# Optimization experiments

Hardware: AMD Instinct MI355X
Metric: run time of the kernel (lower is better)

Reference implementation:

```python
import jax, jax.numpy as jnp
import numpy as np

N = 2800        # real node count (before hardcoded pad)
NPAD = 3000     # module pads node dim to 3000
F_IN = 8192     # node_features
H1 = 256        # dim_h1 (GCLSTM in_channels)
H2 = 128        # GCLSTM out_channels
E = 179200      # edges (avg degree 64)


def setup_inputs() -> dict:
    key = jax.random.key(0)
    ks = jax.random.split(key, 12)
    inp = {
        "x": jax.random.normal(ks[0], (N, F_IN), jnp.float32),
        "edge_index": jax.random.randint(ks[1], (2, E), 0, N, dtype=jnp.int64),
        "edge_weight": jax.random.uniform(ks[2], (E,), jnp.float32),
        "h0": jax.random.normal(ks[3], (NPAD, H2), jnp.float32),
        "c0": jax.random.normal(ks[4], (NPAD, H2), jnp.float32),
        # fc0: node_features -> dim_h1
        "fc0_w": jax.random.normal(ks[5], (F_IN, H1), jnp.float32) / np.float32(np.sqrt(F_IN)),
        "fc0_b": jnp.zeros((H1,), jnp.float32),
        # GCLSTM gate params, stacked over gates [i, f, c, o]
        "Wx": jax.random.normal(ks[6], (4, H1, H2), jnp.float32) / np.float32(np.sqrt(H1)),
        "bg": jnp.zeros((4, H2), jnp.float32),
        # ChebConv (K=2) weights per gate: theta_0, theta_1, bias
        "cw0": jax.random.normal(ks[7], (4, H2, H2), jnp.float32) / np.float32(np.sqrt(H2)),
        "cw1": jax.random.normal(ks[8], (4, H2, H2), jnp.float32) / np.float32(np.sqrt(H2)),
        "cb": jnp.zeros((4, H2), jnp.float32),
        # final fc: 128 -> 1
        "fc_w": jax.random.normal(ks[9], (H2, 1), jnp.float32) / np.float32(np.sqrt(H2)),
        "fc_b": jnp.zeros((1,), jnp.float32),
    }
    return inp


def _cheb_scaled_laplacian(edge_index, edge_weight, num_nodes):
    # ChebConv 'sym' norm with lambda_max=2: L_hat = -D^{-1/2} A D^{-1/2}
    # (diagonal of scaled Laplacian cancels to zero with fill_value=-1 self loops)
    row, col = edge_index[0], edge_index[1]
    deg = jax.ops.segment_sum(edge_weight, row, num_segments=num_nodes)
    dinv = jnp.where(deg > 0, jax.lax.rsqrt(jnp.where(deg > 0, deg, 1.0)), 0.0)
    return -dinv[row] * edge_weight * dinv[col]  # per-edge weight of L_hat


def reference(x, edge_weight, h0, c0, fc0_w, fc0_b, Wx, bg, cw0, cw1, cb,
              fc_w, fc_b, edge_index):
    n_real = x.shape[0]
    # hardcoded zero-padding of node dim to 3000
    xp = jnp.concatenate([x, jnp.zeros((NPAD - n_real, x.shape[1]), x.dtype)], axis=0)
    z = jax.nn.relu(xp @ fc0_w + fc0_b)                       # [3000, 256]

    row, col = edge_index[0], edge_index[1]
    w_hat = _cheb_scaled_laplacian(edge_index, edge_weight, NPAD)
    # Chebyshev T1 term: L_hat @ H  (shared across all four gates)
    T1 = jax.ops.segment_sum(w_hat[:, None] * h0[row], col, num_segments=NPAD)  # [3000,128]

    # all four gate pre-activations at once: X W_x + ChebConv(H) + b
    gates = (jnp.einsum('nf,gfo->gno', z, Wx)
             + jnp.einsum('nd,gdo->gno', h0, cw0)
             + jnp.einsum('nd,gdo->gno', T1, cw1)
             + (bg + cb)[:, None, :])                          # [4, 3000, 128]

    i = jax.nn.sigmoid(gates[0])
    f = jax.nn.sigmoid(gates[1])
    t = jnp.tanh(gates[2])
    o = jax.nn.sigmoid(gates[3])
    c_new = f * c0 + i * t
    h_new = o * jnp.tanh(c_new)                                # [3000, 128]

    out = (jax.nn.relu(h_new) @ fc_w + fc_b)[:, 0]             # squeeze last dim
    out = out[:n_real]                                         # drop padding rows
    return out, h_new
```

## Files before the change

kernel.cpp:

```cpp
#include <hip/hip_runtime.h>
#include <math.h>

#define N_REAL 2800
#define NPAD   3000
#define F_IN   8192
#define H1     256
#define H2     128
#define NE     179200
#define UDIM   512
#define NGATE  512
#define MPAD   3072
#define SPLITK 16
#define KCH    (F_IN / SPLITK)

typedef _Float16 half8_t __attribute__((ext_vector_type(8)));
typedef _Float16 half4_t __attribute__((ext_vector_type(4)));
typedef float    floatx4 __attribute__((ext_vector_type(4)));

__device__ __forceinline__ void async_g2l_16(const _Float16* g, _Float16* l) {
    __builtin_amdgcn_global_load_lds(
        (const __attribute__((address_space(1))) unsigned int*)g,
        (__attribute__((address_space(3))) unsigned int*)l, 16, 0, 0);
}

__global__ __launch_bounds__(256)
void prep_kernel(const float* __restrict__ w, const float* __restrict__ Wx,
                 const float* __restrict__ cw0, const float* __restrict__ cw1,
                 const float* __restrict__ bg, const float* __restrict__ cb,
                 const float* __restrict__ h0,
                 _Float16* __restrict__ wTp, _Float16* __restrict__ Wcp,
                 float* __restrict__ biasv, float* __restrict__ deg,
                 int* __restrict__ counts, _Float16* __restrict__ U16) {
    int b = blockIdx.x;
    if (b < 2048) {
        __shared__ float tile[32][33];
        int k0 = (b & 255) * 32;
        int n0 = (b >> 8) * 32;
        int tx = threadIdx.x & 31, ty = threadIdx.x >> 5;
#pragma unroll
        for (int r = 0; r < 4; r++)
            tile[ty + r * 8][tx] = w[(size_t)(k0 + ty + r * 8) * H1 + n0 + tx];
        __syncthreads();
        int t = threadIdx.x;
        if (t < 128) {
            int u_l = t >> 5;
            int n_l = t & 31;
            half8_t h;
#pragma unroll
            for (int j = 0; j < 8; j++) h[j] = (_Float16)tile[u_l * 8 + j][n_l];
            *(half8_t*)&wTp[(((size_t)(k0 >> 3) + u_l) * H1 + n0 + n_l) * 8] = h;
        }
    } else if (b < 3072) {
        int idx = (b - 2048) * 256 + threadIdx.x;
        if (idx < UDIM * NGATE) {
            int col = idx >> 9;
            int f   = idx & 511;
            int g = col >> 7, o = col & 127;
            float v;
            if (f < H1)            v = Wx[((size_t)g * H1 + f) * H2 + o];
            else if (f < H1 + H2)  v = cw0[((size_t)g * H2 + (f - H1)) * H2 + o];
            else                   v = cw1[((size_t)g * H2 + (f - H1 - H2)) * H2 + o];
            Wcp[(((size_t)(f >> 3)) * NGATE + col) * 8 + (f & 7)] = (_Float16)v;
            if (f == 0) biasv[col] = bg[col] + cb[col];
        }
    } else if (b < 3096) {
        int i = (b - 3072) * 256 + threadIdx.x;
        if (i < NPAD) deg[i] = 0.f;
        else { int j = i - NPAD; if (j < 3072) counts[j] = 0; }
    } else {
        int q = (b - 3096) * 256 + threadIdx.x;
        int m = q >> 5;
        int o4 = (q & 31) * 4;
        half4_t h = {};
        if (m < NPAD) {
            float4 v = *(const float4*)&h0[(size_t)m * H2 + o4];
            h[0] = (_Float16)v.x; h[1] = (_Float16)v.y; h[2] = (_Float16)v.z; h[3] = (_Float16)v.w;
        }
        *(half4_t*)&U16[(size_t)m * UDIM + H1 + o4] = h;
    }
}

__global__ __launch_bounds__(256, 3)
void g1hist_kernel(const float* __restrict__ x, const _Float16* __restrict__ wTp,
                   const int* __restrict__ ei, const float* __restrict__ ew,
                   float* __restrict__ P, float* __restrict__ deg,
                   int* __restrict__ counts) {
    __shared__ __align__(16) _Float16 As[8][64][8];
    __shared__ __align__(16) _Float16 Bs[8][256][8];
    const int b = blockIdx.x;
    const int t = threadIdx.x;
    if (b < 700) {
        int e = b * 256 + t;
        if (e < NE) {
            int r = ei[e];
            int c = ei[NE + e];
            atomicAdd(&deg[r], ew[e]);
            atomicAdd(&counts[c], 1);
        }
        return;
    }
    const int lin = b - 700;
    const int sk  = lin & 15;
    const int mb  = lin >> 4;
    const int wave = t >> 6, lane = t & 63;
    const int l16 = lane & 15, u4 = lane >> 4;
    const int m0 = mb * 64;
    const int kbase = sk * KCH;

    const int arow = t >> 2;
    const int aseg = t & 3;
    const bool avalid = (m0 + arow) < N_REAL;
    const float* agp = x + (size_t)(m0 + arow) * F_IN + kbase + aseg * 16;

    floatx4 acc[4][4] = {};

    float4 a0 = make_float4(0.f, 0.f, 0.f, 0.f), a1 = a0, a2 = a0, a3 = a0;
    if (avalid) {
        a0 = *(const float4*)(agp + 0);
        a1 = *(const float4*)(agp + 4);
        a2 = *(const float4*)(agp + 8);
        a3 = *(const float4*)(agp + 12);
    }

    for (int kk = 0; kk < KCH; kk += 64) {
        const _Float16* bbase = wTp + ((size_t)((kbase + kk) >> 3)) * (H1 * 8);
#pragma unroll
        for (int q = 0; q < 2; q++) {
            int u = wave * 2 + q;
#pragma unroll
            for (int rg = 0; rg < 4; rg++)
                async_g2l_16(bbase + ((size_t)u * H1 + rg * 64 + lane) * 8,
                             &Bs[u][rg * 64 + lane][0]);
        }
        half8_t hlo, hhi;
        hlo[0] = (_Float16)a0.x; hlo[1] = (_Float16)a0.y; hlo[2] = (_Float16)a0.z; hlo[3] = (_Float16)a0.w;
        hlo[4] = (_Float16)a1.x; hlo[5] = (_Float16)a1.y; hlo[6] = (_Float16)a1.z; hlo[7] = (_Float16)a1.w;
        hhi[0] = (_Float16)a2.x; hhi[1] = (_Float16)a2.y; hhi[2] = (_Float16)a2.z; hhi[3] = (_Float16)a2.w;
        hhi[4] = (_Float16)a3.x; hhi[5] = (_Float16)a3.y; hhi[6] = (_Float16)a3.z; hhi[7] = (_Float16)a3.w;
        *(half8_t*)&As[aseg * 2][arow][0]     = hlo;
        *(half8_t*)&As[aseg * 2 + 1][arow][0] = hhi;
        __syncthreads();
        if (kk + 64 < KCH && avalid) {
            a0 = *(const float4*)(agp + kk + 64);
            a1 = *(const float4*)(agp + kk + 68);
            a2 = *(const float4*)(agp + kk + 72);
            a3 = *(const float4*)(agp + kk + 76);
        }
#pragma unroll
        for (int ks = 0; ks < 2; ks++) {
            half8_t a[4], bfr[4];
#pragma unroll
            for (int i = 0; i < 4; i++) a[i] = *(const half8_t*)&As[ks * 4 + u4][i * 16 + l16][0];
#pragma unroll
            for (int j = 0; j < 4; j++) bfr[j] = *(const half8_t*)&Bs[ks * 4 + u4][wave * 64 + j * 16 + l16][0];
#pragma unroll
            for (int i = 0; i < 4; i++)
#pragma unroll
                for (int j = 0; j < 4; j++)
                    acc[i][j] = __builtin_amdgcn_mfma_f32_16x16x32_f16(a[i], bfr[j], acc[i][j], 0, 0, 0);
        }
        __syncthreads();
    }

    float* Pb = P + ((size_t)sk * MPAD + m0) * H1;
#pragma unroll
    for (int i = 0; i < 4; i++)
#pragma unroll
        for (int j = 0; j < 4; j++) {
            int n = wave * 64 + j * 16 + l16;
#pragma unroll
            for (int r = 0; r < 4; r++)
                Pb[(size_t)(i * 16 + u4 * 4 + r) * H1 + n] = acc[i][j][r];
        }
}

__device__ __forceinline__ void zreduce_body(int zb, int t, const float* __restrict__ P,
                                             const float* __restrict__ fc0_b,
                                             _Float16* __restrict__ U16) {
    int q = zb * 256 + t;
    int m = q >> 6;
    int n4 = (q & 63) * 4;
    float s0 = 0.f, s1 = 0.f, s2 = 0.f, s3 = 0.f;
#pragma unroll
    for (int sk = 0; sk < SPLITK; sk++) {
        float4 p = *(const float4*)&P[((size_t)sk * MPAD + m) * H1 + n4];
        s0 += p.x; s1 += p.y; s2 += p.z; s3 += p.w;
    }
    float4 bb = *(const float4*)&fc0_b[n4];
    half4_t h;
    h[0] = (_Float16)fmaxf(s0 + bb.x, 0.f);
    h[1] = (_Float16)fmaxf(s1 + bb.y, 0.f);
    h[2] = (_Float16)fmaxf(s2 + bb.z, 0.f);
    h[3] = (_Float16)fmaxf(s3 + bb.w, 0.f);
    *(half4_t*)&U16[(size_t)m * UDIM + n4] = h;
}

__global__ __launch_bounds__(256)
void scanz_kernel(const int* __restrict__ counts, int* __restrict__ offsets,
                  const float* __restrict__ deg, float* __restrict__ dinv,
                  int* __restrict__ cursor, const float* __restrict__ P,
                  const float* __restrict__ fc0_b, _Float16* __restrict__ U16) {
    int b = blockIdx.x;
    int t = threadIdx.x;
    if (b == 0) {
        __shared__ int wt[4];
        int i0 = t * 12;
        int v[12];
        int s = 0;
#pragma unroll
        for (int j = 0; j < 12; j++) { v[j] = counts[i0 + j]; s += v[j]; }
        int incl = s;
#pragma unroll
        for (int d = 1; d < 64; d <<= 1) {
            int n = __shfl_up(incl, d);
            if ((t & 63) >= d) incl += n;
        }
        if ((t & 63) == 63) wt[t >> 6] = incl;
        __syncthreads();
        int wbase = 0;
#pragma unroll
        for (int w = 0; w < 4; w++) wbase += (w < (t >> 6)) ? wt[w] : 0;
        int run = wbase + incl - s;
#pragma unroll
        for (int j = 0; j < 12; j++) {
            offsets[i0 + j] = run;
            cursor[i0 + j]  = run;
            run += v[j];
        }
        for (int i = t; i < NPAD; i += 256) {
            float d = deg[i];
            dinv[i] = (d > 0.f) ? rsqrtf(d) : 0.f;
        }
    } else {
        zreduce_body(b - 1, t, P, fc0_b, U16);
    }
}

__global__ __launch_bounds__(256)
void scatz_kernel(const int* __restrict__ ei, int* __restrict__ cursor,
                  int* __restrict__ eid, const float* __restrict__ P,
                  const float* __restrict__ fc0_b, _Float16* __restrict__ U16) {
    int b = blockIdx.x;
    int t = threadIdx.x;
    if (b < 700) {
        int e = b * 256 + t;
        if (e < NE) {
            int c = ei[NE + e];
            int p = atomicAdd(&cursor[c], 1);
            eid[p] = e;
        }
    } else {
        zreduce_body(384 + (b - 700), t, P, fc0_b, U16);
    }
}

__global__ __launch_bounds__(128)
void gather_kernel(const int* __restrict__ ei, const float* __restrict__ ew,
                   const float* __restrict__ h0, const float* __restrict__ dinv,
                   const int* __restrict__ offsets, const int* __restrict__ eid,
                   _Float16* __restrict__ U16) {
    __shared__ int   sr[128];
    __shared__ float sw[128];
    int n = blockIdx.x;
    int t = threadIdx.x;
    int beg = offsets[n], end = offsets[n + 1];
    float dc = dinv[n];
    float acc = 0.f;
    for (int base = beg; base < end; base += 128) {
        int j = base + t;
        if (j < end) {
            int e = eid[j];
            int r = ei[e];
            sr[t] = r;
            sw[t] = -dinv[r] * ew[e];
        }
        __syncthreads();
        int cnt = min(128, end - base);
        int k = 0;
        for (; k + 8 <= cnt; k += 8) {
            int   r0 = sr[k],   r1 = sr[k+1], r2 = sr[k+2], r3 = sr[k+3];
            int   r4 = sr[k+4], r5 = sr[k+5], r6 = sr[k+6], r7 = sr[k+7];
            float w0 = sw[k],   w1 = sw[k+1], w2 = sw[k+2], w3 = sw[k+3];
            float w4 = sw[k+4], w5 = sw[k+5], w6 = sw[k+6], w7 = sw[k+7];
            float v0 = h0[(size_t)r0 * H2 + t];
            float v1 = h0[(size_t)r1 * H2 + t];
            float v2 = h0[(size_t)r2 * H2 + t];
            float v3 = h0[(size_t)r3 * H2 + t];
            float v4 = h0[(size_t)r4 * H2 + t];
            float v5 = h0[(size_t)r5 * H2 + t];
            float v6 = h0[(size_t)r6 * H2 + t];
            float v7 = h0[(size_t)r7 * H2 + t];
            acc += w0 * v0 + w1 * v1 + w2 * v2 + w3 * v3
                 + w4 * v4 + w5 * v5 + w6 * v6 + w7 * v7;
        }
        for (; k < cnt; k++)
            acc += sw[k] * h0[(size_t)sr[k] * H2 + t];
        __syncthreads();
    }
    U16[(size_t)n * UDIM + H1 + H2 + t] = (_Float16)(acc * dc);
}

__global__ __launch_bounds__(256, 3)
void gemm2_mfma(const _Float16* __restrict__ U16, const _Float16* __restrict__ Wcp,
                float* __restrict__ gatesP) {
    __shared__ __align__(16) _Float16 As[8][64][8];
    __shared__ __align__(16) _Float16 Bs[8][256][8];
    const int t = threadIdx.x;
    const int wave = t >> 6, lane = t & 63;
    const int l16 = lane & 15, u4 = lane >> 4;
    const int n0 = blockIdx.x * 256;
    const int m0 = blockIdx.y * 64;
    const int kz = blockIdx.z * 256;

    floatx4 acc[4][4] = {};

    for (int kk = kz; kk < kz + 256; kk += 64) {
        const _Float16* bbase = Wcp + ((size_t)(kk >> 3)) * (NGATE * 8);
#pragma unroll
        for (int q = 0; q < 2; q++) {
            int u = wave * 2 + q;
            async_g2l_16(U16 + (size_t)(m0 + lane) * UDIM + kk + u * 8, &As[u][lane][0]);
#pragma unroll
            for (int rg = 0; rg < 4; rg++)
                async_g2l_16(bbase + ((size_t)u * NGATE + n0 + rg * 64 + lane) * 8,
                             &Bs[u][rg * 64 + lane][0]);
        }
        __syncthreads();
#pragma unroll
        for (int ks = 0; ks < 2; ks++) {
            half8_t a[4], bfr[4];
#pragma unroll
            for (int i = 0; i < 4; i++) a[i] = *(const half8_t*)&As[ks * 4 + u4][i * 16 + l16][0];
#pragma unroll
            for (int j = 0; j < 4; j++) bfr[j] = *(const half8_t*)&Bs[ks * 4 + u4][wave * 64 + j * 16 + l16][0];
#pragma unroll
            for (int i = 0; i < 4; i++)
#pragma unroll
                for (int j = 0; j < 4; j++)
                    acc[i][j] = __builtin_amdgcn_mfma_f32_16x16x32_f16(a[i], bfr[j], acc[i][j], 0, 0, 0);
        }
        __syncthreads();
    }

    float* g = gatesP + (size_t)blockIdx.z * MPAD * NGATE;
#pragma unroll
    for (int i = 0; i < 4; i++)
#pragma unroll
        for (int j = 0; j < 4; j++) {
            int n = n0 + wave * 64 + j * 16 + l16;
#pragma unroll
            for (int r = 0; r < 4; r++)
                g[(size_t)(m0 + i * 16 + u4 * 4 + r) * NGATE + n] = acc[i][j][r];
        }
}

__global__ __launch_bounds__(128)
void lstm_kernel(const float* __restrict__ gates, const float* __restrict__ c0,
                 const float* __restrict__ biasv, const float* __restrict__ fc_w,
                 const float* __restrict__ fc_b, float* __restrict__ out) {
    __shared__ float red[2];
    int n = blockIdx.x;
    int o = threadIdx.x;
    const float* g0 = gates + (size_t)n * NGATE;
    const float* g1 = g0 + (size_t)MPAD * NGATE;
    float gi = g0[o]          + g1[o]          + biasv[o];
    float gf = g0[H2 + o]     + g1[H2 + o]     + biasv[H2 + o];
    float gt = g0[2 * H2 + o] + g1[2 * H2 + o] + biasv[2 * H2 + o];
    float go = g0[3 * H2 + o] + g1[3 * H2 + o] + biasv[3 * H2 + o];
    float iv = 1.f / (1.f + expf(-gi));
    float fv = 1.f / (1.f + expf(-gf));
    float tv = tanhf(gt);
    float ov = 1.f / (1.f + expf(-go));
    float c = fv * c0[(size_t)n * H2 + o] + iv * tv;
    float h = ov * tanhf(c);
    out[N_REAL + (size_t)n * H2 + o] = h;

    float r = fmaxf(h, 0.f) * fc_w[o];
#pragma unroll
    for (int s = 32; s; s >>= 1) r += __shfl_down(r, s);
    if ((o & 63) == 0) red[o >> 6] = r;
    __syncthreads();
    if (o == 0 && n < N_REAL) out[n] = red[0] + red[1] + fc_b[0];
}

extern "C" void kernel_launch(void* const* d_in, const int* in_sizes, int n_in,
                              void* d_out, int out_size, void* d_ws, size_t ws_size,
                              hipStream_t stream) {
    const float* x     = (const float*)d_in[0];
    const int*   ei    = (const int*)d_in[1];
    const float* ew    = (const float*)d_in[2];
    const float* h0    = (const float*)d_in[3];
    const float* c0    = (const float*)d_in[4];
    const float* fc0_w = (const float*)d_in[5];
    const float* fc0_b = (const float*)d_in[6];
    const float* Wx    = (const float*)d_in[7];
    const float* bg    = (const float*)d_in[8];
    const float* cw0   = (const float*)d_in[9];
    const float* cw1   = (const float*)d_in[10];
    const float* cb    = (const float*)d_in[11];
    const float* fc_w  = (const float*)d_in[12];
    const float* fc_b  = (const float*)d_in[13];
    float* out = (float*)d_out;

    float* P      = (float*)d_ws;
    float* gates  = P + (size_t)SPLITK * MPAD * H1;
    float* biasv  = gates + 2 * (size_t)MPAD * NGATE;
    float* deg    = biasv + NGATE;
    float* dinv   = deg + NPAD;
    int*   counts = (int*)(dinv + NPAD);
    int*   offs   = counts + 3072;
    int*   cursor = offs + 3072;
    int*   eid    = cursor + 3072;
    _Float16* U16 = (_Float16*)(((uintptr_t)(eid + NE) + 255) & ~(uintptr_t)255);
    _Float16* Wcp = U16 + (size_t)MPAD * UDIM;
    _Float16* wTp = Wcp + (size_t)UDIM * NGATE;

    prep_kernel<<<3480, 256, 0, stream>>>(fc0_w, Wx, cw0, cw1, bg, cb, h0, wTp, Wcp, biasv, deg, counts, U16);
    g1hist_kernel<<<700 + (MPAD / 64) * SPLITK, 256, 0, stream>>>(x, wTp, ei, ew, P, deg, counts);
    scanz_kernel<<<385, 256, 0, stream>>>(counts, offs, deg, dinv, cursor, P, fc0_b, U16);
    scatz_kernel<<<1084, 256, 0, stream>>>(ei, cursor, eid, P, fc0_b, U16);
    gather_kernel<<<NPAD, 128, 0, stream>>>(ei, ew, h0, dinv, offs, eid, U16);
    gemm2_mfma<<<dim3(NGATE / 256, MPAD / 64, 2), 256, 0, stream>>>(U16, Wcp, gates);
    lstm_kernel<<<NPAD, 128, 0, stream>>>(gates, c0, biasv, fc_w, fc_b, out);
}
```

Baseline: 270.2 us.

## Privatize edge histograms in LDS and overlap gather with partial gate GEMM

Degree and count histograms are now built by eight blocks using shared-memory atomics and written out as per-block partials, which removes the deg/counts zeroing and the global atomics. The CSR scatter then uses per-block LDS cursors built from the prefix sums. The gate GEMM is split by K: the z and h0 part (K 0..384) runs in the same launch as the T1 gather, and a small second kernel handles the T1 columns. The gather now uses 256 threads that split the edges into two halves. The risks are that only 8 blocks do the histogram and scatter work, so those phases have little parallelism, and the eid order inside each segment changes.

```diff
diff --git a/kernel.cpp b/kernel.cpp
--- a/kernel.cpp
+++ b/kernel.cpp
@@ -12,10 +12,15 @@
 #define MPAD   3072
 #define SPLITK 16
 #define KCH    (F_IN / SPLITK)
+#define NHB    8
+#define EPB    (NE / NHB)
 
 typedef _Float16 half8_t __attribute__((ext_vector_type(8)));
 typedef _Float16 half4_t __attribute__((ext_vector_type(4)));
 typedef float    floatx4 __attribute__((ext_vector_type(4)));
+
+typedef _Float16 AsT[64][8];
+typedef _Float16 BsT[256][8];
 
 __device__ __forceinline__ void async_g2l_16(const _Float16* g, _Float16* l) {
     __builtin_amdgcn_global_load_lds(
@@ -29,8 +34,7 @@
                  const float* __restrict__ bg, const float* __restrict__ cb,
                  const float* __restrict__ h0,
                  _Float16* __restrict__ wTp, _Float16* __restrict__ Wcp,
-                 float* __restrict__ biasv, float* __restrict__ deg,
-                 int* __restrict__ counts, _Float16* __restrict__ U16) {
+                 float* __restrict__ biasv, _Float16* __restrict__ U16) {
     int b = blockIdx.x;
     if (b < 2048) {
         __shared__ float tile[32][33];
@@ -63,12 +67,8 @@
             Wcp[(((size_t)(f >> 3)) * NGATE + col) * 8 + (f & 7)] = (_Float16)v;
             if (f == 0) biasv[col] = bg[col] + cb[col];
         }
-    } else if (b < 3096) {
-        int i = (b - 3072) * 256 + threadIdx.x;
-        if (i < NPAD) deg[i] = 0.f;
-        else { int j = i - NPAD; if (j < 3072) counts[j] = 0; }
     } else {
-        int q = (b - 3096) * 256 + threadIdx.x;
+        int q = (b - 3072) * 256 + threadIdx.x;
         int m = q >> 5;
         int o4 = (q & 31) * 4;
         half4_t h = {};
@@ -83,23 +83,32 @@
 __global__ __launch_bounds__(256, 3)
 void g1hist_kernel(const float* __restrict__ x, const _Float16* __restrict__ wTp,
                    const int* __restrict__ ei, const float* __restrict__ ew,
-                   float* __restrict__ P, float* __restrict__ deg,
-                   int* __restrict__ counts) {
-    __shared__ __align__(16) _Float16 As[8][64][8];
-    __shared__ __align__(16) _Float16 Bs[8][256][8];
+                   float* __restrict__ P, int* __restrict__ cnt_p,
+                   float* __restrict__ deg_p) {
+    __shared__ __align__(16) char smem[40960];
     const int b = blockIdx.x;
     const int t = threadIdx.x;
-    if (b < 700) {
-        int e = b * 256 + t;
-        if (e < NE) {
-            int r = ei[e];
-            int c = ei[NE + e];
-            atomicAdd(&deg[r], ew[e]);
-            atomicAdd(&counts[c], 1);
+    if (b < NHB) {
+        float* sdeg = (float*)smem;
+        int*   scnt = (int*)(smem + 12288);
+        for (int i = t; i < 3072; i += 256) { sdeg[i] = 0.f; scnt[i] = 0; }
+        __syncthreads();
+        int e0 = b * EPB;
+        for (int i = t; i < EPB; i += 256) {
+            int e = e0 + i;
+            atomicAdd(&sdeg[ei[e]], ew[e]);
+            atomicAdd(&scnt[ei[NE + e]], 1);
+        }
+        __syncthreads();
+        for (int i = t; i < 3072; i += 256) {
+            deg_p[b * 3072 + i] = sdeg[i];
+            cnt_p[b * 3072 + i] = scnt[i];
         }
         return;
     }
-    const int lin = b - 700;
+    AsT* As = reinterpret_cast<AsT*>(smem);
+    BsT* Bs = reinterpret_cast<BsT*>(smem + 8192);
+    const int lin = b - NHB;
     const int sk  = lin & 15;
     const int mb  = lin >> 4;
     const int wave = t >> 6, lane = t & 63;
@@ -196,10 +205,10 @@
 }
 
 __global__ __launch_bounds__(256)
-void scanz_kernel(const int* __restrict__ counts, int* __restrict__ offsets,
-                  const float* __restrict__ deg, float* __restrict__ dinv,
-                  int* __restrict__ cursor, const float* __restrict__ P,
-                  const float* __restrict__ fc0_b, _Float16* __restrict__ U16) {
+void scanz_kernel(const int* __restrict__ cnt_p, const float* __restrict__ deg_p,
+                  int* __restrict__ offsets, float* __restrict__ dinv,
+                  const float* __restrict__ P, const float* __restrict__ fc0_b,
+                  _Float16* __restrict__ U16) {
     int b = blockIdx.x;
     int t = threadIdx.x;
     if (b == 0) {
@@ -208,7 +217,12 @@
         int v[12];
         int s = 0;
 #pragma unroll
-        for (int j = 0; j < 12; j++) { v[j] = counts[i0 + j]; s += v[j]; }
+        for (int j = 0; j < 12; j++) {
+            int tv = 0;
+#pragma unroll
+            for (int bb = 0; bb < NHB; bb++) tv += cnt_p[bb * 3072 + i0 + j];
+            v[j] = tv; s += tv;
+        }
         int incl = s;
 #pragma unroll
         for (int d = 1; d < 64; d <<= 1) {
@@ -222,13 +236,11 @@
         for (int w = 0; w < 4; w++) wbase += (w < (t >> 6)) ? wt[w] : 0;
         int run = wbase + incl - s;
 #pragma unroll
-        for (int j = 0; j < 12; j++) {
-            offsets[i0 + j] = run;
-            cursor[i0 + j]  = run;
-            run += v[j];
-        }
+        for (int j = 0; j < 12; j++) { offsets[i0 + j] = run; run += v[j]; }
         for (int i = t; i < NPAD; i += 256) {
-            float d = deg[i];
+            float d = 0.f;
+#pragma unroll
+            for (int bb = 0; bb < NHB; bb++) d += deg_p[bb * 3072 + i];
             dinv[i] = (d > 0.f) ? rsqrtf(d) : 0.f;
         }
     } else {
@@ -237,36 +249,107 @@
 }
 
 __global__ __launch_bounds__(256)
-void scatz_kernel(const int* __restrict__ ei, int* __restrict__ cursor,
-                  int* __restrict__ eid, const float* __restrict__ P,
-                  const float* __restrict__ fc0_b, _Float16* __restrict__ U16) {
+void scatz_kernel(const int* __restrict__ ei, const int* __restrict__ offsets,
+                  const int* __restrict__ cnt_p, int* __restrict__ eid,
+                  const float* __restrict__ P, const float* __restrict__ fc0_b,
+                  _Float16* __restrict__ U16) {
     int b = blockIdx.x;
     int t = threadIdx.x;
-    if (b < 700) {
-        int e = b * 256 + t;
-        if (e < NE) {
+    if (b < NHB) {
+        __shared__ int sbase[3072];
+        for (int j = t; j < 3072; j += 256) {
+            int a = offsets[j];
+            for (int bb = 0; bb < b; bb++) a += cnt_p[bb * 3072 + j];
+            sbase[j] = a;
+        }
+        __syncthreads();
+        int e0 = b * EPB;
+        for (int i = t; i < EPB; i += 256) {
+            int e = e0 + i;
             int c = ei[NE + e];
-            int p = atomicAdd(&cursor[c], 1);
+            int p = atomicAdd(&sbase[c], 1);
             eid[p] = e;
         }
     } else {
-        zreduce_body(384 + (b - 700), t, P, fc0_b, U16);
-    }
-}
-
-__global__ __launch_bounds__(128)
-void gather_kernel(const int* __restrict__ ei, const float* __restrict__ ew,
-                   const float* __restrict__ h0, const float* __restrict__ dinv,
-                   const int* __restrict__ offsets, const int* __restrict__ eid,
-                   _Float16* __restrict__ U16) {
-    __shared__ int   sr[128];
-    __shared__ float sw[128];
-    int n = blockIdx.x;
+        zreduce_body(384 + (b - NHB), t, P, fc0_b, U16);
+    }
+}
+
+__device__ __forceinline__ void gemm2_body(const _Float16* __restrict__ U16,
+                                           const _Float16* __restrict__ Wcp,
+                                           float* __restrict__ g,
+                                           int k0, int kend, int blk, int t, char* smem) {
+    AsT* As = reinterpret_cast<AsT*>(smem);
+    BsT* Bs = reinterpret_cast<BsT*>(smem + 8192);
+    const int wave = t >> 6, lane = t & 63;
+    const int l16 = lane & 15, u4 = lane >> 4;
+    const int n0 = (blk & 1) * 256;
+    const int m0 = (blk >> 1) * 64;
+
+    floatx4 acc[4][4] = {};
+
+    for (int kk = k0; kk < kend; kk += 64) {
+        const _Float16* bbase = Wcp + ((size_t)(kk >> 3)) * (NGATE * 8);
+#pragma unroll
+        for (int q = 0; q < 2; q++) {
+            int u = wave * 2 + q;
+            async_g2l_16(U16 + (size_t)(m0 + lane) * UDIM + kk + u * 8, &As[u][lane][0]);
+#pragma unroll
+            for (int rg = 0; rg < 4; rg++)
+                async_g2l_16(bbase + ((size_t)u * NGATE + n0 + rg * 64 + lane) * 8,
+                             &Bs[u][rg * 64 + lane][0]);
+        }
+        __syncthreads();
+#pragma unroll
+        for (int ks = 0; ks < 2; ks++) {
+            half8_t a[4], bfr[4];
+#pragma unroll
+            for (int i = 0; i < 4; i++) a[i] = *(const half8_t*)&As[ks * 4 + u4][i * 16 + l16][0];
+#pragma unroll
+            for (int j = 0; j < 4; j++) bfr[j] = *(const half8_t*)&Bs[ks * 4 + u4][wave * 64 + j * 16 + l16][0];
+#pragma unroll
+            for (int i = 0; i < 4; i++)
+#pragma unroll
+                for (int j = 0; j < 4; j++)
+                    acc[i][j] = __builtin_amdgcn_mfma_f32_16x16x32_f16(a[i], bfr[j], acc[i][j], 0, 0, 0);
+        }
+        __syncthreads();
+    }
+
+#pragma unroll
+    for (int i = 0; i < 4; i++)
+#pragma unroll
+        for (int j = 0; j < 4; j++) {
+            int n = n0 + wave * 64 + j * 16 + l16;
+#pragma unroll
+            for (int r = 0; r < 4; r++)
+                g[(size_t)(m0 + i * 16 + u4 * 4 + r) * NGATE + n] = acc[i][j][r];
+        }
+}
+
+__global__ __launch_bounds__(256, 3)
+void g2gather_kernel(const _Float16* __restrict__ U16f, _Float16* __restrict__ U16,
+                     const _Float16* __restrict__ Wcp, float* __restrict__ gates,
+                     const int* __restrict__ ei, const float* __restrict__ ew,
+                     const float* __restrict__ h0, const float* __restrict__ dinv,
+                     const int* __restrict__ offsets, const int* __restrict__ eid) {
+    __shared__ __align__(16) char smem[40960];
+    int b = blockIdx.x;
     int t = threadIdx.x;
+    if (b < 96) {
+        gemm2_body(U16f, Wcp, gates, 0, 384, b, t, smem);
+        return;
+    }
+    int*   sr = (int*)smem;
+    float* sw = (float*)(smem + 1024);
+    float* sa = (float*)(smem + 2048);
+    int n = b - 96;
+    int o = t & 127;
+    int g = t >> 7;
     int beg = offsets[n], end = offsets[n + 1];
     float dc = dinv[n];
     float acc = 0.f;
-    for (int base = beg; base < end; base += 128) {
+    for (int base = beg; base < end; base += 256) {
         int j = base + t;
         if (j < end) {
             int e = eid[j];
@@ -275,83 +358,41 @@
             sw[t] = -dinv[r] * ew[e];
         }
         __syncthreads();
-        int cnt = min(128, end - base);
-        int k = 0;
-        for (; k + 8 <= cnt; k += 8) {
+        int cnt = min(256, end - base);
+        int lo = g * 128;
+        int hi = min(cnt, lo + 128);
+        int k = lo;
+        for (; k + 8 <= hi; k += 8) {
             int   r0 = sr[k],   r1 = sr[k+1], r2 = sr[k+2], r3 = sr[k+3];
             int   r4 = sr[k+4], r5 = sr[k+5], r6 = sr[k+6], r7 = sr[k+7];
             float w0 = sw[k],   w1 = sw[k+1], w2 = sw[k+2], w3 = sw[k+3];
             float w4 = sw[k+4], w5 = sw[k+5], w6 = sw[k+6], w7 = sw[k+7];
-            float v0 = h0[(size_t)r0 * H2 + t];
-            float v1 = h0[(size_t)r1 * H2 + t];
-            float v2 = h0[(size_t)r2 * H2 + t];
-            float v3 = h0[(size_t)r3 * H2 + t];
-            float v4 = h0[(size_t)r4 * H2 + t];
-            float v5 = h0[(size_t)r5 * H2 + t];
-            float v6 = h0[(size_t)r6 * H2 + t];
-            float v7 = h0[(size_t)r7 * H2 + t];
+            float v0 = h0[(size_t)r0 * H2 + o];
+            float v1 = h0[(size_t)r1 * H2 + o];
+            float v2 = h0[(size_t)r2 * H2 + o];
+            float v3 = h0[(size_t)r3 * H2 + o];
+            float v4 = h0[(size_t)r4 * H2 + o];
+            float v5 = h0[(size_t)r5 * H2 + o];
+            float v6 = h0[(size_t)r6 * H2 + o];
+            float v7 = h0[(size_t)r7 * H2 + o];
             acc += w0 * v0 + w1 * v1 + w2 * v2 + w3 * v3
                  + w4 * v4 + w5 * v5 + w6 * v6 + w7 * v7;
         }
-        for (; k < cnt; k++)
-            acc += sw[k] * h0[(size_t)sr[k] * H2 + t];
-        __syncthreads();
-    }
-    U16[(size_t)n * UDIM + H1 + H2 + t] = (_Float16)(acc * dc);
+        for (; k < hi; k++)
+            acc += sw[k] * h0[(size_t)sr[k] * H2 + o];
+        __syncthreads();
+    }
+    sa[t] = acc;
+    __syncthreads();
+    if (g == 0)
+        U16[(size_t)n * UDIM + H1 + H2 + o] = (_Float16)((acc + sa[t + 128]) * dc);
 }
 
 __global__ __launch_bounds__(256, 3)
-void gemm2_mfma(const _Float16* __restrict__ U16, const _Float16* __restrict__ Wcp,
-                float* __restrict__ gatesP) {
-    __shared__ __align__(16) _Float16 As[8][64][8];
-    __shared__ __align__(16) _Float16 Bs[8][256][8];
-    const int t = threadIdx.x;
-    const int wave = t >> 6, lane = t & 63;
-    const int l16 = lane & 15, u4 = lane >> 4;
-    const int n0 = blockIdx.x * 256;
-    const int m0 = blockIdx.y * 64;
-    const int kz = blockIdx.z * 256;
-
-    floatx4 acc[4][4] = {};
-
-    for (int kk = kz; kk < kz + 256; kk += 64) {
-        const _Float16* bbase = Wcp + ((size_t)(kk >> 3)) * (NGATE * 8);
-#pragma unroll
-        for (int q = 0; q < 2; q++) {
-            int u = wave * 2 + q;
-            async_g2l_16(U16 + (size_t)(m0 + lane) * UDIM + kk + u * 8, &As[u][lane][0]);
-#pragma unroll
-            for (int rg = 0; rg < 4; rg++)
-                async_g2l_16(bbase + ((size_t)u * NGATE + n0 + rg * 64 + lane) * 8,
-                             &Bs[u][rg * 64 + lane][0]);
-        }
-        __syncthreads();
-#pragma unroll
-        for (int ks = 0; ks < 2; ks++) {
-            half8_t a[4], bfr[4];
-#pragma unroll
-            for (int i = 0; i < 4; i++) a[i] = *(const half8_t*)&As[ks * 4 + u4][i * 16 + l16][0];
-#pragma unroll
-            for (int j = 0; j < 4; j++) bfr[j] = *(const half8_t*)&Bs[ks * 4 + u4][wave * 64 + j * 16 + l16][0];
-#pragma unroll
-            for (int i = 0; i < 4; i++)
-#pragma unroll
-                for (int j = 0; j < 4; j++)
-                    acc[i][j] = __builtin_amdgcn_mfma_f32_16x16x32_f16(a[i], bfr[j], acc[i][j], 0, 0, 0);
-        }
-        __syncthreads();
-    }
-
-    float* g = gatesP + (size_t)blockIdx.z * MPAD * NGATE;
-#pragma unroll
-    for (int i = 0; i < 4; i++)
-#pragma unroll
-        for (int j = 0; j < 4; j++) {
-            int n = n0 + wave * 64 + j * 16 + l16;
-#pragma unroll
-            for (int r = 0; r < 4; r++)
-                g[(size_t)(m0 + i * 16 + u4 * 4 + r) * NGATE + n] = acc[i][j][r];
-        }
+void gemm2b_kernel(const _Float16* __restrict__ U16, const _Float16* __restrict__ Wcp,
+                   float* __restrict__ gates) {
+    __shared__ __align__(16) char smem[40960];
+    gemm2_body(U16, Wcp, gates + (size_t)MPAD * NGATE, 384, 512, blockIdx.x, threadIdx.x, smem);
 }
 
 __global__ __launch_bounds__(128)
@@ -405,21 +446,20 @@
     float* P      = (float*)d_ws;
     float* gates  = P + (size_t)SPLITK * MPAD * H1;
     float* biasv  = gates + 2 * (size_t)MPAD * NGATE;
-    float* deg    = biasv + NGATE;
-    float* dinv   = deg + NPAD;
-    int*   counts = (int*)(dinv + NPAD);
-    int*   offs   = counts + 3072;
-    int*   cursor = offs + 3072;
-    int*   eid    = cursor + 3072;
-    _Float16* U16 = (_Float16*)(((uintptr_t)(eid + NE) + 255) & ~(uintptr_t)255);
+    float* dinv   = biasv + NGATE;
+    int*   offs   = (int*)(dinv + 3072);
+    int*   cnt_p  = offs + 3072;
+    int*   eid    = cnt_p + NHB * 3072;
+    float* deg_p  = (float*)(eid + NE);
+    _Float16* U16 = (_Float16*)(((uintptr_t)(deg_p + NHB * 3072) + 255) & ~(uintptr_t)255);
     _Float16* Wcp = U16 + (size_t)MPAD * UDIM;
     _Float16* wTp = Wcp + (size_t)UDIM * NGATE;
 
-    prep_kernel<<<3480, 256, 0, stream>>>(fc0_w, Wx, cw0, cw1, bg, cb, h0, wTp, Wcp, biasv, deg, counts, U16);
-    g1hist_kernel<<<700 + (MPAD / 64) * SPLITK, 256, 0, stream>>>(x, wTp, ei, ew, P, deg, counts);
-    scanz_kernel<<<385, 256, 0, stream>>>(counts, offs, deg, dinv, cursor, P, fc0_b, U16);
-    scatz_kernel<<<1084, 256, 0, stream>>>(ei, cursor, eid, P, fc0_b, U16);
-    gather_kernel<<<NPAD, 128, 0, stream>>>(ei, ew, h0, dinv, offs, eid, U16);
-    gemm2_mfma<<<dim3(NGATE / 256, MPAD / 64, 2), 256, 0, stream>>>(U16, Wcp, gates);
+    prep_kernel<<<3456, 256, 0, stream>>>(fc0_w, Wx, cw0, cw1, bg, cb, h0, wTp, Wcp, biasv, U16);
+    g1hist_kernel<<<NHB + (MPAD / 64) * SPLITK, 256, 0, stream>>>(x, wTp, ei, ew, P, cnt_p, deg_p);
+    scanz_kernel<<<385, 256, 0, stream>>>(cnt_p, deg_p, offs, dinv, P, fc0_b, U16);
+    scatz_kernel<<<NHB + 384, 256, 0, stream>>>(ei, offs, cnt_p, eid, P, fc0_b, U16);
+    g2gather_kernel<<<96 + NPAD, 256, 0, stream>>>(U16, U16, Wcp, gates, ei, ew, h0, dinv, offs, eid);
+    gemm2b_kernel<<<96, 256, 0, stream>>>(U16, Wcp, gates);
     lstm_kernel<<<NPAD, 128, 0, stream>>>(gates, c0, biasv, fc_w, fc_b, out);
 }
```

New measurement: 335.7 us. 24.3% more time.

## Build edge histogram and CSR scatter with per-block LDS counters

Applied to the files above, without the earlier changes.

The degree and column-count histogram moves out of the GEMM1 kernel into prep_kernel, where 64 blocks each accumulate a private LDS histogram. Each block then flushes it to global memory with one atomic per bin and records its per-bin counts. A per-bin prefix over blocks gives every block its own base offsets, so the scatter step uses LDS atomics instead of contended global cursor atomics. This aims to cut global atomic traffic and free the GEMM1 launch of histogram blocks, at the cost of an extra memset and more workspace. Within each bin, the order of edges in the CSR now follows block order and LDS atomic arrival order rather than global atomic arrival order.

```diff
diff --git a/kernel.cpp b/kernel.cpp
--- a/kernel.cpp
+++ b/kernel.cpp
@@ -12,6 +12,8 @@
 #define MPAD   3072
 #define SPLITK 16
 #define KCH    (F_IN / SPLITK)
+#define NHB    64
+#define EPB    (NE / NHB)
 
 typedef _Float16 half8_t __attribute__((ext_vector_type(8)));
 typedef _Float16 half4_t __attribute__((ext_vector_type(4)));
@@ -27,21 +29,42 @@
 void prep_kernel(const float* __restrict__ w, const float* __restrict__ Wx,
                  const float* __restrict__ cw0, const float* __restrict__ cw1,
                  const float* __restrict__ bg, const float* __restrict__ cb,
-                 const float* __restrict__ h0,
+                 const float* __restrict__ h0, const int* __restrict__ ei,
+                 const float* __restrict__ ew,
                  _Float16* __restrict__ wTp, _Float16* __restrict__ Wcp,
-                 float* __restrict__ biasv, float* __restrict__ deg,
-                 int* __restrict__ counts, _Float16* __restrict__ U16) {
+                 float* __restrict__ biasv, _Float16* __restrict__ U16,
+                 float* __restrict__ deg, int* __restrict__ counts,
+                 int* __restrict__ cnt_pT) {
+    __shared__ __align__(16) char pmem[24576];
     int b = blockIdx.x;
-    if (b < 2048) {
-        __shared__ float tile[32][33];
-        int k0 = (b & 255) * 32;
-        int n0 = (b >> 8) * 32;
-        int tx = threadIdx.x & 31, ty = threadIdx.x >> 5;
+    int t = threadIdx.x;
+    if (b < NHB) {
+        float* sdeg = (float*)pmem;
+        int*   scnt = (int*)(pmem + 12288);
+        for (int i = t; i < 3072; i += 256) { sdeg[i] = 0.f; scnt[i] = 0; }
+        __syncthreads();
+        int e0 = b * EPB;
+        for (int i = t; i < EPB; i += 256) {
+            int e = e0 + i;
+            atomicAdd(&sdeg[ei[e]], ew[e]);
+            atomicAdd(&scnt[ei[NE + e]], 1);
+        }
+        __syncthreads();
+        for (int i = t; i < 3072; i += 256) {
+            atomicAdd(&deg[i], sdeg[i]);
+            atomicAdd(&counts[i], scnt[i]);
+            cnt_pT[i * NHB + b] = scnt[i];
+        }
+    } else if (b < 2112) {
+        float (*tile)[33] = (float(*)[33])pmem;
+        int bb = b - NHB;
+        int k0 = (bb & 255) * 32;
+        int n0 = (bb >> 8) * 32;
+        int tx = t & 31, ty = t >> 5;
 #pragma unroll
         for (int r = 0; r < 4; r++)
             tile[ty + r * 8][tx] = w[(size_t)(k0 + ty + r * 8) * H1 + n0 + tx];
         __syncthreads();
-        int t = threadIdx.x;
         if (t < 128) {
             int u_l = t >> 5;
             int n_l = t & 31;
@@ -50,8 +73,8 @@
             for (int j = 0; j < 8; j++) h[j] = (_Float16)tile[u_l * 8 + j][n_l];
             *(half8_t*)&wTp[(((size_t)(k0 >> 3) + u_l) * H1 + n0 + n_l) * 8] = h;
         }
-    } else if (b < 3072) {
-        int idx = (b - 2048) * 256 + threadIdx.x;
+    } else if (b < 3136) {
+        int idx = (b - 2112) * 256 + t;
         if (idx < UDIM * NGATE) {
             int col = idx >> 9;
             int f   = idx & 511;
@@ -63,12 +86,8 @@
             Wcp[(((size_t)(f >> 3)) * NGATE + col) * 8 + (f & 7)] = (_Float16)v;
             if (f == 0) biasv[col] = bg[col] + cb[col];
         }
-    } else if (b < 3096) {
-        int i = (b - 3072) * 256 + threadIdx.x;
-        if (i < NPAD) deg[i] = 0.f;
-        else { int j = i - NPAD; if (j < 3072) counts[j] = 0; }
     } else {
-        int q = (b - 3096) * 256 + threadIdx.x;
+        int q = (b - 3136) * 256 + t;
         int m = q >> 5;
         int o4 = (q & 31) * 4;
         half4_t h = {};
@@ -81,31 +100,15 @@
 }
 
 __global__ __launch_bounds__(256, 3)
-void g1hist_kernel(const float* __restrict__ x, const _Float16* __restrict__ wTp,
-                   const int* __restrict__ ei, const float* __restrict__ ew,
-                   float* __restrict__ P, float* __restrict__ deg,
-                   int* __restrict__ counts) {
+void gemm1_fused(const float* __restrict__ x, const _Float16* __restrict__ wTp,
+                 float* __restrict__ P) {
     __shared__ __align__(16) _Float16 As[8][64][8];
     __shared__ __align__(16) _Float16 Bs[8][256][8];
-    const int b = blockIdx.x;
     const int t = threadIdx.x;
-    if (b < 700) {
-        int e = b * 256 + t;
-        if (e < NE) {
-            int r = ei[e];
-            int c = ei[NE + e];
-            atomicAdd(&deg[r], ew[e]);
-            atomicAdd(&counts[c], 1);
-        }
-        return;
-    }
-    const int lin = b - 700;
-    const int sk  = lin & 15;
-    const int mb  = lin >> 4;
     const int wave = t >> 6, lane = t & 63;
     const int l16 = lane & 15, u4 = lane >> 4;
-    const int m0 = mb * 64;
-    const int kbase = sk * KCH;
+    const int m0 = blockIdx.x * 64;
+    const int kbase = blockIdx.y * KCH;
 
     const int arow = t >> 2;
     const int aseg = t & 3;
@@ -162,7 +165,7 @@
         __syncthreads();
     }
 
-    float* Pb = P + ((size_t)sk * MPAD + m0) * H1;
+    float* Pb = P + ((size_t)blockIdx.y * MPAD + m0) * H1;
 #pragma unroll
     for (int i = 0; i < 4; i++)
 #pragma unroll
@@ -196,10 +199,11 @@
 }
 
 __global__ __launch_bounds__(256)
-void scanz_kernel(const int* __restrict__ counts, int* __restrict__ offsets,
-                  const float* __restrict__ deg, float* __restrict__ dinv,
-                  int* __restrict__ cursor, const float* __restrict__ P,
-                  const float* __restrict__ fc0_b, _Float16* __restrict__ U16) {
+void scanz_kernel(const int* __restrict__ counts, const float* __restrict__ deg,
+                  int* __restrict__ offsets, float* __restrict__ dinv,
+                  const int* __restrict__ cnt_pT, int* __restrict__ base_rel,
+                  const float* __restrict__ P, const float* __restrict__ fc0_b,
+                  _Float16* __restrict__ U16) {
     int b = blockIdx.x;
     int t = threadIdx.x;
     if (b == 0) {
@@ -222,35 +226,44 @@
         for (int w = 0; w < 4; w++) wbase += (w < (t >> 6)) ? wt[w] : 0;
         int run = wbase + incl - s;
 #pragma unroll
-        for (int j = 0; j < 12; j++) {
-            offsets[i0 + j] = run;
-            cursor[i0 + j]  = run;
-            run += v[j];
-        }
+        for (int j = 0; j < 12; j++) { offsets[i0 + j] = run; run += v[j]; }
         for (int i = t; i < NPAD; i += 256) {
             float d = deg[i];
             dinv[i] = (d > 0.f) ? rsqrtf(d) : 0.f;
         }
+    } else if (b <= 12) {
+        int j = (b - 1) * 256 + t;
+        const int* src = cnt_pT + (size_t)j * NHB;
+        int* dst = base_rel + (size_t)j * NHB;
+        int run = 0;
+#pragma unroll
+        for (int bb = 0; bb < NHB; bb++) { dst[bb] = run; run += src[bb]; }
     } else {
-        zreduce_body(b - 1, t, P, fc0_b, U16);
+        zreduce_body(b - 13, t, P, fc0_b, U16);
     }
 }
 
 __global__ __launch_bounds__(256)
-void scatz_kernel(const int* __restrict__ ei, int* __restrict__ cursor,
-                  int* __restrict__ eid, const float* __restrict__ P,
-                  const float* __restrict__ fc0_b, _Float16* __restrict__ U16) {
+void scatz_kernel(const int* __restrict__ ei, const int* __restrict__ offsets,
+                  const int* __restrict__ base_rel, int* __restrict__ eid,
+                  const float* __restrict__ P, const float* __restrict__ fc0_b,
+                  _Float16* __restrict__ U16) {
     int b = blockIdx.x;
     int t = threadIdx.x;
-    if (b < 700) {
-        int e = b * 256 + t;
-        if (e < NE) {
+    if (b < NHB) {
+        __shared__ int sb[3072];
+        for (int j = t; j < 3072; j += 256)
+            sb[j] = offsets[j] + base_rel[(size_t)j * NHB + b];
+        __syncthreads();
+        int e0 = b * EPB;
+        for (int i = t; i < EPB; i += 256) {
+            int e = e0 + i;
             int c = ei[NE + e];
-            int p = atomicAdd(&cursor[c], 1);
+            int p = atomicAdd(&sb[c], 1);
             eid[p] = e;
         }
     } else {
-        zreduce_body(384 + (b - 700), t, P, fc0_b, U16);
+        zreduce_body(384 + (b - NHB), t, P, fc0_b, U16);
     }
 }
 
@@ -402,23 +415,26 @@
     const float* fc_b  = (const float*)d_in[13];
     float* out = (float*)d_out;
 
-    float* P      = (float*)d_ws;
-    float* gates  = P + (size_t)SPLITK * MPAD * H1;
-    float* biasv  = gates + 2 * (size_t)MPAD * NGATE;
-    float* deg    = biasv + NGATE;
-    float* dinv   = deg + NPAD;
-    int*   counts = (int*)(dinv + NPAD);
-    int*   offs   = counts + 3072;
-    int*   cursor = offs + 3072;
-    int*   eid    = cursor + 3072;
+    float* P        = (float*)d_ws;
+    float* gates    = P + (size_t)SPLITK * MPAD * H1;
+    float* biasv    = gates + 2 * (size_t)MPAD * NGATE;
+    float* dinv     = biasv + NGATE;
+    float* deg      = dinv + 3072;
+    int*   counts   = (int*)(deg + 3072);
+    int*   offs     = counts + 3072;
+    int*   cnt_pT   = offs + 3072;
+    int*   base_rel = cnt_pT + 3072 * NHB;
+    int*   eid      = base_rel + 3072 * NHB;
     _Float16* U16 = (_Float16*)(((uintptr_t)(eid + NE) + 255) & ~(uintptr_t)255);
     _Float16* Wcp = U16 + (size_t)MPAD * UDIM;
     _Float16* wTp = Wcp + (size_t)UDIM * NGATE;
 
-    prep_kernel<<<3480, 256, 0, stream>>>(fc0_w, Wx, cw0, cw1, bg, cb, h0, wTp, Wcp, biasv, deg, counts, U16);
-    g1hist_kernel<<<700 + (MPAD / 64) * SPLITK, 256, 0, stream>>>(x, wTp, ei, ew, P, deg, counts);
-    scanz_kernel<<<385, 256, 0, stream>>>(counts, offs, deg, dinv, cursor, P, fc0_b, U16);
-    scatz_kernel<<<1084, 256, 0, stream>>>(ei, cursor, eid, P, fc0_b, U16);
+    hipMemsetAsync(deg, 0, 2 * 3072 * sizeof(float), stream);
+    prep_kernel<<<3520, 256, 0, stream>>>(fc0_w, Wx, cw0, cw1, bg, cb, h0, ei, ew,
+                                          wTp, Wcp, biasv, U16, deg, counts, cnt_pT);
+    gemm1_fused<<<dim3(MPAD / 64, SPLITK), 256, 0, stream>>>(x, wTp, P);
+    scanz_kernel<<<397, 256, 0, stream>>>(counts, deg, offs, dinv, cnt_pT, base_rel, P, fc0_b, U16);
+    scatz_kernel<<<NHB + 384, 256, 0, stream>>>(ei, offs, base_rel, eid, P, fc0_b, U16);
     gather_kernel<<<NPAD, 128, 0, stream>>>(ei, ew, h0, dinv, offs, eid, U16);
     gemm2_mfma<<<dim3(NGATE / 256, MPAD / 64, 2), 256, 0, stream>>>(U16, Wcp, gates);
     lstm_kernel<<<NPAD, 128, 0, stream>>>(gates, c0, biasv, fc_w, fc_b, out);
```

New measurement: 242.9 us. 1.11x faster.
